# Performance work log

Measured on AMD Instinct MI355X. Metric: run time of the kernel, lower is better.

## Reference

```python
import math
import jax, jax.numpy as jnp
import numpy as np
from jax import lax

B, H, W, C1, D, NH = 32, 28, 28, 64, 256, 8
KS, RATIO = 9, 0.0005
NEG = -1.0e9


def setup_inputs() -> dict:
    key = jax.random.key(0)
    ks = jax.random.split(key, 6)
    x = jax.random.normal(ks[0], (B, 1, H, W), jnp.float32)
    conv_w = jax.random.normal(ks[1], (C1, 1, KS, KS), jnp.float32) * 0.05
    channel_embed = jax.random.normal(ks[2], (C1, D), jnp.float32)
    in_proj_w = jax.random.normal(ks[3], (3 * D, D), jnp.float32) * (1.0 / math.sqrt(D))
    in_proj_b = jnp.zeros((3 * D,), jnp.float32)
    out_proj_w = jax.random.normal(ks[4], (D, D), jnp.float32) * (1.0 / math.sqrt(D))
    out_proj_b = jnp.zeros((D,), jnp.float32)
    return {"x": x, "conv_w": conv_w, "channel_embed": channel_embed,
            "in_proj_w": in_proj_w, "in_proj_b": in_proj_b,
            "out_proj_w": out_proj_w, "out_proj_b": out_proj_b}


def _pos_encoding_2d(h, w, dim):
    # even dims: sin(y * div), odd dims: cos(x * div)  (matches torch broadcast)
    div = jnp.exp(jnp.arange(0, dim, 2, dtype=jnp.float32) * (-math.log(10000.0) / dim))
    pe_even = jnp.sin(jnp.arange(h, dtype=jnp.float32)[:, None] * div)  # (h, dim/2)
    pe_odd = jnp.cos(jnp.arange(w, dtype=jnp.float32)[:, None] * div)   # (w, dim/2)
    pe = jnp.zeros((h, w, dim), jnp.float32)
    pe = pe.at[..., 0::2].set(jnp.broadcast_to(pe_even[:, None, :], (h, w, dim // 2)))
    pe = pe.at[..., 1::2].set(jnp.broadcast_to(pe_odd[None, :, :], (h, w, dim // 2)))
    return pe


def reference(x, conv_w, channel_embed, in_proj_w, in_proj_b, out_proj_w, out_proj_b):
    pad = KS // 2
    A = jax.nn.relu(lax.conv_general_dilated(
        x, conv_w, (1, 1), [(pad, pad), (pad, pad)],
        dimension_numbers=("NCHW", "OIHW", "NCHW")))  # (B, C1, H, W)

    # global top-k threshold (kthvalue equivalent)
    total = A.size
    k = max(1, int(math.ceil(RATIO * total)))
    if k >= total:
        mask_global = jnp.ones_like(A, dtype=bool)
    else:
        vals, _ = lax.top_k(A.reshape(-1), k)
        mask_global = A >= vals[-1]
    A_g = A * mask_global.astype(A.dtype)

    v = jnp.transpose(A_g, (0, 2, 3, 1))  # (B, H, W, C1)
    nz = v > 0
    count = nz.sum(axis=-1)  # (B, H, W)

    top2_vals, top2_idx = lax.top_k(v, 2)  # (B,H,W,2)
    cidx = jnp.arange(C1)
    sel2 = (cidx == top2_idx[..., 0:1]) | (cidx == top2_idx[..., 1:2])
    idx_single = jnp.argmax(jnp.where(nz, v, -jnp.inf), axis=-1)
    sel1 = cidx == idx_single[..., None]

    logits = jnp.where((count >= 2)[..., None] & sel2, v, NEG)
    logits = jnp.where((count == 1)[..., None] & sel1, v, logits)
    sparse_weights = jax.nn.softmax(logits, axis=-1)
    sparse_weights = jnp.where((count == 0)[..., None], 0.0, sparse_weights)

    loc_emb = jnp.einsum("bhwc,cd->bhwd", sparse_weights, channel_embed)
    loc_emb = loc_emb + _pos_encoding_2d(H, W, D)[None]
    seq = loc_emb.reshape(B, H * W, D)

    # torch nn.MultiheadAttention (batch_first, self-attn)
    qkv = seq @ in_proj_w.T + in_proj_b  # (B, S, 3D)
    q, kk, vv = jnp.split(qkv, 3, axis=-1)
    hd = D // NH
    def heads(t):
        return t.reshape(B, H * W, NH, hd).transpose(0, 2, 1, 3)  # (B, NH, S, hd)
    q, kk, vv = heads(q), heads(kk), heads(vv)
    scores = jnp.einsum("bnqd,bnkd->bnqk", q, kk) / math.sqrt(hd)
    attn = jax.nn.softmax(scores, axis=-1)
    ctx = jnp.einsum("bnqk,bnkd->bnqd", attn, vv)
    ctx = ctx.transpose(0, 2, 1, 3).reshape(B, H * W, D)
    attn_out = ctx @ out_proj_w.T + out_proj_b
    pooled = attn_out.mean(axis=1)  # (B, D)
    return pooled, sparse_weights, top2_idx
```

## Files before the change

### kernel.cpp

```cpp
#include <hip/hip_runtime.h>
#include <cmath>

#define NB 32
#define C1N 64
#define DIM 256
#define NHEAD 8
#define SEQL 784
#define NA 1605632
#define SEQN 6422528
#define KSEL 803u
#define QK2S (0.17677669529663687f * 1.4426950408889634f)
#define THR2 11.541560f
#define PECOEF (-0.03597789207803197f)

#define AS1 __attribute__((address_space(1)))
#define AS3 __attribute__((address_space(3)))

typedef __attribute__((ext_vector_type(8))) short bf16x8;
typedef __attribute__((ext_vector_type(4))) float f32x4;

__device__ __forceinline__ unsigned short f2b(float f) {
  unsigned u = __float_as_uint(f);
  unsigned r = u + 0x7fffu + ((u >> 16) & 1u);
  return (unsigned short)(r >> 16);
}

__device__ __forceinline__ unsigned cvt_pk_bf16(float lo, float hi) {
  unsigned r;
  asm("v_cvt_pk_bf16_f32 %0, %1, %2" : "=v"(r) : "v"(lo), "v"(hi));
  return r;
}

__device__ __forceinline__ void scan256_suffix(unsigned* ss, int t) {
  #pragma unroll
  for (int off = 1; off < 256; off <<= 1) {
    unsigned v = (t + off < 256) ? ss[t + off] : 0u;
    __syncthreads();
    ss[t] += v;
    __syncthreads();
  }
}

__global__ __launch_bounds__(256) void k_init(const float* __restrict__ ipw,
                                              unsigned short* __restrict__ wbuf,
                                              unsigned* __restrict__ z) {
  int i = blockIdx.x * 256 + threadIdx.x;
  if (i < 66080) z[i] = 0u;
  wbuf[i] = f2b(ipw[i]);
}

__global__ __launch_bounds__(256) void k_conv(const float* __restrict__ x,
                                              const float* __restrict__ cw,
                                              float* __restrict__ vbuf,
                                              unsigned* __restrict__ hist8a) {
  __shared__ __align__(16) float ximg[1296];
  __shared__ float wlds[5184];
  __shared__ unsigned lh[256];
  int tid = threadIdx.x;
  int b = blockIdx.x / 7, sblk = blockIdx.x % 7;
  lh[tid] = 0u;
  for (int e = tid; e < 1296; e += 256) ximg[e] = 0.f;
  for (int e = tid; e < 5184; e += 256) {
    int c = e / 81, t = e - c * 81;
    wlds[t * 64 + c] = cw[e];
  }
  __syncthreads();
  const float* xb = x + b * 784;
  for (int e = tid; e < 784; e += 256) {
    int row = e / 28, col = e - row * 28;
    ximg[(row + 4) * 36 + col + 4] = xb[e];
  }
  __syncthreads();
  int wv = tid >> 6, lane = tid & 63;
  for (int it = 0; it < 7; ++it) {
    int grp = sblk * 28 + it * 4 + wv;
    int hr = grp / 7, wc0 = (grp % 7) * 4;
    float a0 = 0.f, a1 = 0.f, a2 = 0.f, a3 = 0.f;
    #pragma unroll
    for (int dy = 0; dy < 9; ++dy) {
      const float4* xr4 = (const float4*)&ximg[(hr + dy) * 36 + wc0];
      float4 xa = xr4[0], xbq = xr4[1], xc = xr4[2];
      float xr[12] = {xa.x, xa.y, xa.z, xa.w, xbq.x, xbq.y, xbq.z, xbq.w,
                      xc.x, xc.y, xc.z, xc.w};
      #pragma unroll
      for (int dx = 0; dx < 9; ++dx) {
        float w = wlds[(dy * 9 + dx) * 64 + lane];
        a0 = fmaf(xr[dx + 0], w, a0);
        a1 = fmaf(xr[dx + 1], w, a1);
        a2 = fmaf(xr[dx + 2], w, a2);
        a3 = fmaf(xr[dx + 3], w, a3);
      }
    }
    a0 = fmaxf(a0, 0.f); a1 = fmaxf(a1, 0.f);
    a2 = fmaxf(a2, 0.f); a3 = fmaxf(a3, 0.f);
    size_t base = ((size_t)(b * 784 + hr * 28 + wc0)) * 64 + lane;
    vbuf[base +   0] = a0;
    vbuf[base +  64] = a1;
    vbuf[base + 128] = a2;
    vbuf[base + 192] = a3;
    if (a0 > 0.f) atomicAdd(&lh[__float_as_uint(a0) >> 24], 1u);
    if (a1 > 0.f) atomicAdd(&lh[__float_as_uint(a1) >> 24], 1u);
    if (a2 > 0.f) atomicAdd(&lh[__float_as_uint(a2) >> 24], 1u);
    if (a3 > 0.f) atomicAdd(&lh[__float_as_uint(a3) >> 24], 1u);
  }
  __syncthreads();
  if (lh[tid] > 0u) atomicAdd(&hist8a[tid], lh[tid]);
}

__global__ __launch_bounds__(256) void k_h8b(const float* __restrict__ vbuf,
                                             const unsigned* __restrict__ hist8a,
                                             unsigned* __restrict__ hist8b) {
  __shared__ unsigned ss[256];
  __shared__ unsigned lh[256];
  __shared__ unsigned bkey;
  int t = threadIdx.x;
  ss[t] = hist8a[t];
  lh[t] = 0u;
  __syncthreads();
  scan256_suffix(ss, t);
  if (ss[0] < KSEL) return;
  unsigned S = ss[t], ab = (t < 255) ? ss[t + 1] : 0u;
  if (S >= KSEL && ab < KSEL) bkey = (unsigned)t;
  __syncthreads();
  unsigned key = bkey;
  const float4* v4 = (const float4*)vbuf;
  int n4 = NA / 4;
  for (int i = blockIdx.x * 256 + t; i < n4; i += gridDim.x * 256) {
    float4 v = v4[i];
    float vv[4] = {v.x, v.y, v.z, v.w};
    #pragma unroll
    for (int j = 0; j < 4; ++j) {
      if (vv[j] > 0.0f) {
        unsigned bits = __float_as_uint(vv[j]);
        if ((bits >> 24) == key) atomicAdd(&lh[(bits >> 16) & 0xFFu], 1u);
      }
    }
  }
  __syncthreads();
  if (lh[t] > 0u) atomicAdd(&hist8b[t], lh[t]);
}

__global__ __launch_bounds__(256) void k_h16(const float* __restrict__ vbuf,
                                             const unsigned* __restrict__ hist8a,
                                             const unsigned* __restrict__ hist8b,
                                             unsigned* __restrict__ hist16) {
  __shared__ unsigned ss[256];
  __shared__ unsigned bk0, bk1, brem;
  int t = threadIdx.x;
  ss[t] = hist8a[t];
  __syncthreads();
  scan256_suffix(ss, t);
  if (ss[0] < KSEL) return;
  unsigned S = ss[t], ab = (t < 255) ? ss[t + 1] : 0u;
  if (S >= KSEL && ab < KSEL) { bk0 = (unsigned)t; brem = KSEL - ab; }
  __syncthreads();
  unsigned key0 = bk0, rem1 = brem;
  __syncthreads();
  ss[t] = hist8b[t];
  __syncthreads();
  scan256_suffix(ss, t);
  S = ss[t]; ab = (t < 255) ? ss[t + 1] : 0u;
  if (S >= rem1 && ab < rem1) bk1 = (unsigned)t;
  __syncthreads();
  unsigned key16 = (key0 << 8) | bk1;
  const float4* v4 = (const float4*)vbuf;
  int n4 = NA / 4;
  for (int i = blockIdx.x * 256 + t; i < n4; i += gridDim.x * 256) {
    float4 v = v4[i];
    float vv[4] = {v.x, v.y, v.z, v.w};
    #pragma unroll
    for (int j = 0; j < 4; ++j) {
      if (vv[j] > 0.0f) {
        unsigned bits = __float_as_uint(vv[j]);
        if ((bits >> 16) == key16) atomicAdd(&hist16[bits & 0xFFFFu], 1u);
      }
    }
  }
}

__global__ __launch_bounds__(1024) void k_scan16(const unsigned* __restrict__ hist8a,
                                                 const unsigned* __restrict__ hist8b,
                                                 const unsigned* __restrict__ hist16,
                                                 unsigned* __restrict__ sel) {
  __shared__ unsigned ss[1024];
  __shared__ unsigned bk0, bk1, brem, brem2;
  int t = threadIdx.x;
  if (t < 256) ss[t] = hist8a[t];
  __syncthreads();
  for (int off = 1; off < 256; off <<= 1) {
    unsigned v = 0u;
    if (t < 256) v = (t + off < 256) ? ss[t + off] : 0u;
    __syncthreads();
    if (t < 256) ss[t] += v;
    __syncthreads();
  }
  if (ss[0] < KSEL) { if (t == 0) sel[3] = 0u; return; }
  if (t < 256) {
    unsigned S = ss[t], ab = (t < 255) ? ss[t + 1] : 0u;
    if (S >= KSEL && ab < KSEL) { bk0 = (unsigned)t; brem = KSEL - ab; }
  }
  __syncthreads();
  unsigned key0 = bk0, rem1 = brem;
  if (t < 256) ss[t] = hist8b[t];
  __syncthreads();
  for (int off = 1; off < 256; off <<= 1) {
    unsigned v = 0u;
    if (t < 256) v = (t + off < 256) ? ss[t + off] : 0u;
    __syncthreads();
    if (t < 256) ss[t] += v;
    __syncthreads();
  }
  if (t < 256) {
    unsigned S = ss[t], ab = (t < 255) ? ss[t + 1] : 0u;
    if (S >= rem1 && ab < rem1) { bk1 = (unsigned)t; brem2 = rem1 - ab; }
  }
  __syncthreads();
  unsigned key16 = (key0 << 8) | bk1;
  unsigned rem2 = brem2;
  unsigned sum = 0;
  for (int i = 0; i < 64; ++i) sum += hist16[t * 64 + i];
  ss[t] = sum;
  __syncthreads();
  for (int off = 1; off < 1024; off <<= 1) {
    unsigned v = (t + off < 1024) ? ss[t + off] : 0u;
    __syncthreads();
    ss[t] += v;
    __syncthreads();
  }
  unsigned S = ss[t];
  unsigned above = (t < 1023) ? ss[t + 1] : 0u;
  if (S >= rem2 && above < rem2) {
    unsigned cum = above;
    for (int bb = t * 64 + 63; bb >= t * 64; --bb) {
      unsigned hb = hist16[bb];
      cum += hb;
      if (cum >= rem2) {
        sel[3] = (key16 << 16) | (unsigned)bb;
        break;
      }
    }
  }
}

__global__ __launch_bounds__(256) void k_select(const float* __restrict__ vbuf,
                                                const unsigned* __restrict__ sel,
                                                const float* __restrict__ ce,
                                                unsigned short* __restrict__ seqb,
                                                float* __restrict__ out_sw,
                                                float* __restrict__ out_idx) {
  int wid = threadIdx.x >> 6;
  int lane = threadIdx.x & 63;
  int pos = blockIdx.x * 4 + wid;
  int hw = pos % 784;
  int hr = hw / 28;
  int wc = hw % 28;
  float thr = __uint_as_float(sel[3]);
  float a = vbuf[(size_t)pos * 64 + lane];
  float val = (a >= thr) ? a : 0.0f;
  unsigned long long nzm = __ballot(val > 0.0f);
  int count = __popcll(nzm);
  float v1 = val; int i1 = lane;
  #pragma unroll
  for (int off = 32; off > 0; off >>= 1) {
    float ov = __shfl_xor(v1, off);
    int oi = __shfl_xor(i1, off);
    if (ov > v1 || (ov == v1 && oi < i1)) { v1 = ov; i1 = oi; }
  }
  float vx = (lane == i1) ? -INFINITY : val;
  float v2 = vx; int i2 = lane;
  #pragma unroll
  for (int off = 32; off > 0; off >>= 1) {
    float ov = __shfl_xor(v2, off);
    int oi = __shfl_xor(i2, off);
    if (ov > v2 || (ov == v2 && oi < i2)) { v2 = ov; i2 = oi; }
  }
  float w1 = 0.0f, w2 = 0.0f;
  if (count >= 2) {
    float e = __expf(v2 - v1);
    float invd = 1.0f / (1.0f + e);
    w1 = invd; w2 = e * invd;
  } else if (count == 1) {
    w1 = 1.0f;
  }
  float wt = (lane == i1) ? w1 : ((lane == i2) ? w2 : 0.0f);
  out_sw[(size_t)pos * 64 + lane] = wt;
  if (lane < 2) out_idx[pos * 2 + lane] = (float)(lane == 0 ? i1 : i2);
  int d0 = lane * 4;
  float4 c1v = *(const float4*)(ce + (size_t)i1 * 256 + d0);
  float4 c2v = *(const float4*)(ce + (size_t)i2 * 256 + d0);
  float dv0 = __expf((float)d0 * PECOEF);
  float dv2 = __expf((float)(d0 + 2) * PECOEF);
  float ox = w1 * c1v.x + w2 * c2v.x + __sinf((float)hr * dv0);
  float oy = w1 * c1v.y + w2 * c2v.y + __cosf((float)wc * dv0);
  float oz = w1 * c1v.z + w2 * c2v.z + __sinf((float)hr * dv2);
  float ow = w1 * c1v.w + w2 * c2v.w + __cosf((float)wc * dv2);
  ushort4 ob = make_ushort4(f2b(ox), f2b(oy), f2b(oz), f2b(ow));
  *(ushort4*)(seqb + (size_t)pos * 256 + d0) = ob;
}

__global__ __launch_bounds__(256) void k_gemm_lds(const unsigned short* __restrict__ A,
                                                  const unsigned short* __restrict__ W,
                                                  const float* __restrict__ bias,
                                                  unsigned short* __restrict__ C,
                                                  unsigned short* __restrict__ Vt,
                                                  int M, int N, int K) {
  __shared__ __align__(16) unsigned short As[8192];
  __shared__ __align__(16) unsigned short Bs[8192];
  int tid = threadIdx.x;
  int lane = tid & 63, wid = tid >> 6;
  int q = lane & 15, g = lane >> 4;
  int m0 = blockIdx.y * 128, n0 = blockIdx.x * 128;
  int lrow = lane >> 3, s = lane & 7;
  const unsigned short* aSrc = A + (size_t)(m0 + wid * 8 + lrow) * K + (s ^ lrow) * 8;
  const unsigned short* bSrc = W + (size_t)(n0 + wid * 8 + lrow) * K + (s ^ lrow) * 8;
  int dstW = wid * 512;
  int mloc = (wid >> 1) * 64, nloc = (wid & 1) * 64;
  int q7 = q & 7;
  f32x4 acc[4][4];
  #pragma unroll
  for (int i = 0; i < 4; ++i)
    #pragma unroll
    for (int j = 0; j < 4; ++j) acc[i][j] = (f32x4){0.f, 0.f, 0.f, 0.f};
  for (int k0 = 0; k0 < K; k0 += 64) {
    #pragma unroll
    for (int i = 0; i < 4; ++i) {
      __builtin_amdgcn_global_load_lds((const AS1 void*)(aSrc + (size_t)i * 32 * K + k0),
                                       (AS3 void*)(&As[i * 2048 + dstW]), 16, 0, 0);
      __builtin_amdgcn_global_load_lds((const AS1 void*)(bSrc + (size_t)i * 32 * K + k0),
                                       (AS3 void*)(&Bs[i * 2048 + dstW]), 16, 0, 0);
    }
    __syncthreads();
    #pragma unroll
    for (int kk = 0; kk < 2; ++kk) {
      bf16x8 af[4], bf[4];
      #pragma unroll
      for (int i = 0; i < 4; ++i)
        af[i] = *(const bf16x8*)&As[(mloc + i * 16 + q) * 64 + (((kk * 4 + g) ^ q7) * 8)];
      #pragma unroll
      for (int j = 0; j < 4; ++j)
        bf[j] = *(const bf16x8*)&Bs[(nloc + j * 16 + q) * 64 + (((kk * 4 + g) ^ q7) * 8)];
      __builtin_amdgcn_s_setprio(1);
      #pragma unroll
      for (int i = 0; i < 4; ++i)
        #pragma unroll
        for (int j = 0; j < 4; ++j)
          acc[i][j] = __builtin_amdgcn_mfma_f32_16x16x32_bf16(af[i], bf[j], acc[i][j], 0, 0, 0);
      __builtin_amdgcn_s_setprio(0);
    }
    __syncthreads();
  }
  if (n0 < 512) {
    #pragma unroll
    for (int j = 0; j < 4; ++j) {
      int col = n0 + nloc + j * 16 + q;
      float bj = bias[col];
      float qs = (col < 256) ? QK2S : 1.0f;
      #pragma unroll
      for (int i = 0; i < 4; ++i) {
        #pragma unroll
        for (int r = 0; r < 4; ++r) {
          int row = m0 + mloc + i * 16 + g * 4 + r;
          C[(size_t)row * N + col] = f2b((acc[i][j][r] + bj) * qs);
        }
      }
    }
  } else {
    #pragma unroll
    for (int j = 0; j < 4; ++j) {
      int colV = n0 + nloc + j * 16 + q;
      float bj = bias[colV];
      int dtot = colV - 512;
      size_t vrow = ((size_t)(dtot >> 5) * 32 + (dtot & 31)) * 800;
      #pragma unroll
      for (int i = 0; i < 4; ++i) {
        int rowbase = m0 + mloc + i * 16;
        int b = rowbase / 784;
        int t16 = rowbase - b * 784;
        int pos = ((t16 >> 5) << 5) + ((t16 >> 4) & 1) * 4 + g * 8;
        uint2 o;
        o.x = cvt_pk_bf16(acc[i][j][0] + bj, acc[i][j][1] + bj);
        o.y = cvt_pk_bf16(acc[i][j][2] + bj, acc[i][j][3] + bj);
        *(uint2*)(Vt + (size_t)b * 8 * 32 * 800 + vrow + pos) = o;
      }
    }
  }
}

__global__ __launch_bounds__(256) void k_attn(const unsigned short* __restrict__ qkv,
                                              const unsigned short* __restrict__ Vt,
                                              unsigned short* __restrict__ ctx) {
  __shared__ __align__(16) unsigned short Kt[3][1024];
  __shared__ __align__(16) unsigned short Vti[3][1024];
  int wid = threadIdx.x >> 6;
  int lane = threadIdx.x & 63;
  int blk = blockIdx.x;
  int wrk = (blk & 7) * 416 + (blk >> 3);
  int bh = wrk / 13;
  int qb = (wrk - bh * 13) * 4 + wid;
  int b = bh >> 3, nh = bh & 7;
  int q = lane & 15, g = lane >> 4;
  bool active = (qb < 49);
  const f32x4 zero4 = {0.f, 0.f, 0.f, 0.f};

  int qrow = b * 784 + (active ? qb * 16 + q : q);
  bf16x8 qf = *(const bf16x8*)(qkv + (size_t)qrow * 768 + nh * 32 + g * 8);
  asm volatile("s_waitcnt vmcnt(0)" ::: "memory");

  const unsigned short* kbase = qkv + (size_t)b * 784 * 768 + 256 + nh * 32;
  const unsigned short* vbase = Vt + (size_t)bh * 32 * 800;

  int rit = ((wid & 1) << 4) + (lane >> 2);
  int sG = (lane & 3) ^ ((rit + (rit >> 2)) & 3);
  bool isK = (wid < 2);
  int ldsoff = ((wid & 1) << 4) * 32;
  const unsigned short* sp = isK ? (kbase + (size_t)rit * 768 + sG * 8)
                                 : (vbase + (size_t)rit * 800 + sG * 8);
  const int sstride = isK ? (32 * 768) : 32;
  unsigned short* ldsb = (isK ? &Kt[0][0] : &Vti[0][0]) + ldsoff;

  int slotr = ((g ^ ((q + (q >> 2)) & 3)) << 3);
  int rowA = q * 32 + slotr;
  int rowB = (16 + q) * 32 + slotr;

  f32x4 acc0 = zero4, acc1 = zero4;
  float m = -INFINITY, lp = 0.f;

#define STAGE(BUFO) {                                                          \
    __builtin_amdgcn_global_load_lds((const AS1 void*)sp,                      \
                                     (AS3 void*)(ldsb + (BUFO)), 16, 0, 0);    \
    sp += sstride; }

#define STEP(CUR, NXT) {                                                       \
    asm volatile("s_waitcnt vmcnt(1)" ::: "memory");                           \
    __builtin_amdgcn_s_barrier();                                              \
    asm volatile("" ::: "memory");                                             \
    STAGE(NXT);                                                                \
    bf16x8 kA = *(const bf16x8*)&Kt[0][(CUR) + rowA];                          \
    bf16x8 kB = *(const bf16x8*)&Kt[0][(CUR) + rowB];                          \
    bf16x8 va = *(const bf16x8*)&Vti[0][(CUR) + rowA];                         \
    bf16x8 vb = *(const bf16x8*)&Vti[0][(CUR) + rowB];                         \
    __builtin_amdgcn_s_setprio(1);                                             \
    f32x4 s0 = __builtin_amdgcn_mfma_f32_16x16x32_bf16(kA, qf, zero4, 0, 0, 0);\
    f32x4 s1 = __builtin_amdgcn_mfma_f32_16x16x32_bf16(kB, qf, zero4, 0, 0, 0);\
    __builtin_amdgcn_s_setprio(0);                                             \
    float pl = fmaxf(fmaxf(fmaxf(s0[0], s0[1]), fmaxf(s0[2], s0[3])),          \
                     fmaxf(fmaxf(s1[0], s1[1]), fmaxf(s1[2], s1[3])));         \
    if (!__all(pl <= m + THR2)) {                                              \
      float pm = fmaxf(pl, __shfl_xor(pl, 16));                                \
      pm = fmaxf(pm, __shfl_xor(pm, 32));                                      \
      float mnew = fmaxf(m, pm);                                               \
      float sc = __builtin_amdgcn_exp2f(m - mnew);                             \
      lp *= sc; acc0 *= sc; acc1 *= sc;                                        \
      m = mnew;                                                                \
    }                                                                          \
    float p0[4], p1[4];                                                        \
    _Pragma("unroll")                                                          \
    for (int r = 0; r < 4; ++r) {                                              \
      p0[r] = __builtin_amdgcn_exp2f(s0[r] - m);                               \
      p1[r] = __builtin_amdgcn_exp2f(s1[r] - m);                               \
    }                                                                          \
    lp += ((p0[0] + p0[1]) + (p0[2] + p0[3]))                                  \
        + ((p1[0] + p1[1]) + (p1[2] + p1[3]));                                 \
    union { unsigned u[4]; bf16x8 v; } pu;                                     \
    pu.u[0] = cvt_pk_bf16(p0[0], p0[1]);                                       \
    pu.u[1] = cvt_pk_bf16(p0[2], p0[3]);                                       \
    pu.u[2] = cvt_pk_bf16(p1[0], p1[1]);                                       \
    pu.u[3] = cvt_pk_bf16(p1[2], p1[3]);                                       \
    __builtin_amdgcn_s_setprio(1);                                             \
    acc0 = __builtin_amdgcn_mfma_f32_16x16x32_bf16(va, pu.v, acc0, 0, 0, 0);   \
    acc1 = __builtin_amdgcn_mfma_f32_16x16x32_bf16(vb, pu.v, acc1, 0, 0, 0);   \
    __builtin_amdgcn_s_setprio(0);                                             \
  }

  STAGE(0);
  STAGE(1024);

  for (int t = 0; t < 8; ++t) {
    STEP(0, 2048);
    STEP(1024, 0);
    STEP(2048, 1024);
  }
  {
    asm volatile("s_waitcnt vmcnt(1)" ::: "memory");
    __builtin_amdgcn_s_barrier();
    asm volatile("" ::: "memory");
    bf16x8 kA = *(const bf16x8*)&Kt[0][rowA];
    bf16x8 va = *(const bf16x8*)&Vti[0][rowA];
    bf16x8 vb = *(const bf16x8*)&Vti[0][rowB];
    f32x4 s0 = __builtin_amdgcn_mfma_f32_16x16x32_bf16(kA, qf, zero4, 0, 0, 0);
    float pl = fmaxf(fmaxf(s0[0], s0[1]), fmaxf(s0[2], s0[3]));
    if (!__all(pl <= m + THR2)) {
      float pm = fmaxf(pl, __shfl_xor(pl, 16));
      pm = fmaxf(pm, __shfl_xor(pm, 32));
      float mnew = fmaxf(m, pm);
      float sc = __builtin_amdgcn_exp2f(m - mnew);
      lp *= sc; acc0 *= sc; acc1 *= sc;
      m = mnew;
    }
    float p0[4];
    #pragma unroll
    for (int r = 0; r < 4; ++r) p0[r] = __builtin_amdgcn_exp2f(s0[r] - m);
    lp += (p0[0] + p0[1]) + (p0[2] + p0[3]);
    union { unsigned u[4]; bf16x8 v; } pu;
    pu.u[0] = cvt_pk_bf16(p0[0], p0[1]);
    pu.u[1] = cvt_pk_bf16(p0[2], p0[3]);
    pu.u[2] = 0u;
    pu.u[3] = 0u;
    acc0 = __builtin_amdgcn_mfma_f32_16x16x32_bf16(va, pu.v, acc0, 0, 0, 0);
    acc1 = __builtin_amdgcn_mfma_f32_16x16x32_bf16(vb, pu.v, acc1, 0, 0, 0);
  }
#undef STEP
#undef STAGE
  float l = lp + __shfl_xor(lp, 16);
  l += __shfl_xor(l, 32);
  float linv = 1.f / l;
  if (active) {
    unsigned short* cp = ctx + (size_t)(b * 784 + qb * 16 + q) * 256 + nh * 32;
    ushort4 oA = make_ushort4(f2b(acc0[0] * linv), f2b(acc0[1] * linv),
                              f2b(acc0[2] * linv), f2b(acc0[3] * linv));
    ushort4 oB = make_ushort4(f2b(acc1[0] * linv), f2b(acc1[1] * linv),
                              f2b(acc1[2] * linv), f2b(acc1[3] * linv));
    *(ushort4*)(cp + g * 4) = oA;
    *(ushort4*)(cp + 16 + g * 4) = oB;
  }
}

__global__ __launch_bounds__(256) void k_poolctx(const unsigned short* __restrict__ ctx,
                                                 float* __restrict__ part) {
  int b = blockIdx.x >> 3, sseg = blockIdx.x & 7;
  int d = threadIdx.x;
  const unsigned short* base = ctx + ((size_t)b * 784 + sseg * 98) * 256 + d;
  float acc = 0.f;
  for (int t = 0; t < 98; ++t)
    acc += __uint_as_float((unsigned)base[(size_t)t * 256] << 16);
  part[(size_t)blockIdx.x * 256 + d] = acc;
}

__global__ __launch_bounds__(256) void k_pgemv(const float* __restrict__ part,
                                               const float* __restrict__ opw,
                                               const float* __restrict__ opb,
                                               float* __restrict__ out) {
  __shared__ float mc[256];
  int b = blockIdx.x, d = threadIdx.x;
  float s = 0.f;
  #pragma unroll
  for (int i = 0; i < 8; ++i) s += part[(size_t)(b * 8 + i) * 256 + d];
  mc[d] = s * (1.0f / 784.0f);
  __syncthreads();
  float acc = opb[d];
  const float4* wr = (const float4*)(opw + (size_t)d * 256);
  #pragma unroll 8
  for (int j = 0; j < 64; ++j) {
    float4 w = wr[j];
    float4 m4 = *(const float4*)&mc[j * 4];
    acc += m4.x * w.x + m4.y * w.y + m4.z * w.z + m4.w * w.w;
  }
  out[b * 256 + d] = acc;
}

extern "C" void kernel_launch(void* const* d_in, const int* in_sizes, int n_in,
                              void* d_out, int out_size, void* d_ws, size_t ws_size,
                              hipStream_t stream) {
  (void)in_sizes; (void)n_in; (void)out_size; (void)ws_size;
  const float* x   = (const float*)d_in[0];
  const float* cw  = (const float*)d_in[1];
  const float* ce  = (const float*)d_in[2];
  const float* ipw = (const float*)d_in[3];
  const float* ipb = (const float*)d_in[4];
  const float* opw = (const float*)d_in[5];
  const float* opb = (const float*)d_in[6];

  float* out = (float*)d_out;
  float* pooled  = out;
  float* out_sw  = out + 8192;
  float* out_idx = out + 8192 + NA;

  float* ws = (float*)d_ws;
  float* vbuf = ws;
  unsigned* hist16 = (unsigned*)(ws + NA);
  unsigned* hist8a = hist16 + 65536;
  unsigned* hist8b = hist8a + 256;
  unsigned* sel    = hist8b + 256;
  unsigned short* seqb = (unsigned short*)(ws + NA + 66080);
  unsigned short* qkvb = seqb + SEQN;
  unsigned short* Vt   = qkvb + 3 * (size_t)SEQN;
  unsigned short* wbuf = Vt + 256 * 32 * 800;
  float* part = (float*)(wbuf + 262144);

  k_init<<<768, 256, 0, stream>>>(ipw, wbuf, hist16);
  k_conv<<<224, 256, 0, stream>>>(x, cw, vbuf, hist8a);
  k_h8b<<<1024, 256, 0, stream>>>(vbuf, hist8a, hist8b);
  k_h16<<<1024, 256, 0, stream>>>(vbuf, hist8a, hist8b, hist16);
  k_scan16<<<1, 1024, 0, stream>>>(hist8a, hist8b, hist16, sel);
  k_select<<<25088 / 4, 256, 0, stream>>>(vbuf, sel, ce, seqb, out_sw, out_idx);
  {
    dim3 gq(768 / 128, 25088 / 128);
    k_gemm_lds<<<gq, 256, 0, stream>>>(seqb, wbuf, ipb, qkvb, Vt, 25088, 768, 256);
  }
  k_attn<<<3328, 256, 0, stream>>>(qkvb, Vt, seqb );
  k_poolctx<<<256, 256, 0, stream>>>(seqb, part);
  k_pgemv<<<NB, 256, 0, stream>>>(part, opw, opb, pooled);
}
```

Before: 164.8 us.

## Compute softmax row sums via MFMA with ones and fuse pooling with output GEMV

In the attention kernel the per-lane scalar sum of probabilities and its final cross-lane shuffles are replaced by an extra MFMA against an all-ones bf16 vector, so the denominator comes out of the matrix unit already reduced. The max computation is also reordered into a shallower three-way form. The separate pooling and output-GEMV kernels are merged into one 1024-thread-per-batch kernel that reduces across segments through shared memory, saving a launch and a workspace round trip. The row sum is now taken from bf16-rounded probabilities, which slightly changes numerics. The fused kernel also runs only 32 blocks, which lowers parallelism in the pooling read.

```diff
diff --git a/kernel.cpp b/kernel.cpp
--- a/kernel.cpp
+++ b/kernel.cpp
@@ -401,6 +401,9 @@
   int q = lane & 15, g = lane >> 4;
   bool active = (qb < 49);
   const f32x4 zero4 = {0.f, 0.f, 0.f, 0.f};
+  const short one_bf = (short)0x3F80;
+  const bf16x8 ones8 = {one_bf, one_bf, one_bf, one_bf,
+                        one_bf, one_bf, one_bf, one_bf};
 
   int qrow = b * 784 + (active ? qb * 16 + q : q);
   bf16x8 qf = *(const bf16x8*)(qkv + (size_t)qrow * 768 + nh * 32 + g * 8);
@@ -422,8 +425,8 @@
   int rowA = q * 32 + slotr;
   int rowB = (16 + q) * 32 + slotr;
 
-  f32x4 acc0 = zero4, acc1 = zero4;
-  float m = -INFINITY, lp = 0.f;
+  f32x4 acc0 = zero4, acc1 = zero4, accS = zero4;
+  float m = -INFINITY;
 
 #define STAGE(BUFO) {                                                          \
     __builtin_amdgcn_global_load_lds((const AS1 void*)sp,                      \
@@ -443,14 +446,16 @@
     f32x4 s0 = __builtin_amdgcn_mfma_f32_16x16x32_bf16(kA, qf, zero4, 0, 0, 0);\
     f32x4 s1 = __builtin_amdgcn_mfma_f32_16x16x32_bf16(kB, qf, zero4, 0, 0, 0);\
     __builtin_amdgcn_s_setprio(0);                                             \
-    float pl = fmaxf(fmaxf(fmaxf(s0[0], s0[1]), fmaxf(s0[2], s0[3])),          \
-                     fmaxf(fmaxf(s1[0], s1[1]), fmaxf(s1[2], s1[3])));         \
+    float t1 = fmaxf(fmaxf(s0[0], s0[1]), s0[2]);                              \
+    float t2 = fmaxf(fmaxf(s0[3], s1[0]), s1[1]);                              \
+    float t3 = fmaxf(fmaxf(s1[2], s1[3]), t1);                                 \
+    float pl = fmaxf(t2, t3);                                                  \
     if (!__all(pl <= m + THR2)) {                                              \
       float pm = fmaxf(pl, __shfl_xor(pl, 16));                                \
       pm = fmaxf(pm, __shfl_xor(pm, 32));                                      \
       float mnew = fmaxf(m, pm);                                               \
       float sc = __builtin_amdgcn_exp2f(m - mnew);                             \
-      lp *= sc; acc0 *= sc; acc1 *= sc;                                        \
+      acc0 *= sc; acc1 *= sc; accS *= sc;                                      \
       m = mnew;                                                                \
     }                                                                          \
     float p0[4], p1[4];                                                        \
@@ -459,8 +464,6 @@
       p0[r] = __builtin_amdgcn_exp2f(s0[r] - m);                               \
       p1[r] = __builtin_amdgcn_exp2f(s1[r] - m);                               \
     }                                                                          \
-    lp += ((p0[0] + p0[1]) + (p0[2] + p0[3]))                                  \
-        + ((p1[0] + p1[1]) + (p1[2] + p1[3]));                                 \
     union { unsigned u[4]; bf16x8 v; } pu;                                     \
     pu.u[0] = cvt_pk_bf16(p0[0], p0[1]);                                       \
     pu.u[1] = cvt_pk_bf16(p0[2], p0[3]);                                       \
@@ -469,6 +472,7 @@
     __builtin_amdgcn_s_setprio(1);                                             \
     acc0 = __builtin_amdgcn_mfma_f32_16x16x32_bf16(va, pu.v, acc0, 0, 0, 0);   \
     acc1 = __builtin_amdgcn_mfma_f32_16x16x32_bf16(vb, pu.v, acc1, 0, 0, 0);   \
+    accS = __builtin_amdgcn_mfma_f32_16x16x32_bf16(ones8, pu.v, accS, 0, 0, 0);\
     __builtin_amdgcn_s_setprio(0);                                             \
   }
 
@@ -488,19 +492,18 @@
     bf16x8 va = *(const bf16x8*)&Vti[0][rowA];
     bf16x8 vb = *(const bf16x8*)&Vti[0][rowB];
     f32x4 s0 = __builtin_amdgcn_mfma_f32_16x16x32_bf16(kA, qf, zero4, 0, 0, 0);
-    float pl = fmaxf(fmaxf(s0[0], s0[1]), fmaxf(s0[2], s0[3]));
+    float pl = fmaxf(fmaxf(fmaxf(s0[0], s0[1]), s0[2]), s0[3]);
     if (!__all(pl <= m + THR2)) {
       float pm = fmaxf(pl, __shfl_xor(pl, 16));
       pm = fmaxf(pm, __shfl_xor(pm, 32));
       float mnew = fmaxf(m, pm);
       float sc = __builtin_amdgcn_exp2f(m - mnew);
-      lp *= sc; acc0 *= sc; acc1 *= sc;
+      acc0 *= sc; acc1 *= sc; accS *= sc;
       m = mnew;
     }
     float p0[4];
     #pragma unroll
     for (int r = 0; r < 4; ++r) p0[r] = __builtin_amdgcn_exp2f(s0[r] - m);
-    lp += (p0[0] + p0[1]) + (p0[2] + p0[3]);
     union { unsigned u[4]; bf16x8 v; } pu;
     pu.u[0] = cvt_pk_bf16(p0[0], p0[1]);
     pu.u[1] = cvt_pk_bf16(p0[2], p0[3]);
@@ -508,12 +511,11 @@
     pu.u[3] = 0u;
     acc0 = __builtin_amdgcn_mfma_f32_16x16x32_bf16(va, pu.v, acc0, 0, 0, 0);
     acc1 = __builtin_amdgcn_mfma_f32_16x16x32_bf16(vb, pu.v, acc1, 0, 0, 0);
+    accS = __builtin_amdgcn_mfma_f32_16x16x32_bf16(ones8, pu.v, accS, 0, 0, 0);
   }
 #undef STEP
 #undef STAGE
-  float l = lp + __shfl_xor(lp, 16);
-  l += __shfl_xor(l, 32);
-  float linv = 1.f / l;
+  float linv = 1.f / accS[0];
   if (active) {
     unsigned short* cp = ctx + (size_t)(b * 784 + qb * 16 + q) * 256 + nh * 32;
     ushort4 oA = make_ushort4(f2b(acc0[0] * linv), f2b(acc0[1] * linv),
@@ -525,37 +527,36 @@
   }
 }
 
-__global__ __launch_bounds__(256) void k_poolctx(const unsigned short* __restrict__ ctx,
-                                                 float* __restrict__ part) {
-  int b = blockIdx.x >> 3, sseg = blockIdx.x & 7;
-  int d = threadIdx.x;
-  const unsigned short* base = ctx + ((size_t)b * 784 + sseg * 98) * 256 + d;
+__global__ __launch_bounds__(1024) void k_poolgemv(const unsigned short* __restrict__ ctx,
+                                                   const float* __restrict__ opw,
+                                                   const float* __restrict__ opb,
+                                                   float* __restrict__ out) {
+  __shared__ float red[4][256];
+  __shared__ float mc[256];
+  int b = blockIdx.x;
+  int d = threadIdx.x & 255;
+  int seg = threadIdx.x >> 8;
+  const unsigned short* base = ctx + ((size_t)b * 784 + seg * 196) * 256 + d;
   float acc = 0.f;
-  for (int t = 0; t < 98; ++t)
+  for (int t = 0; t < 196; ++t)
     acc += __uint_as_float((unsigned)base[(size_t)t * 256] << 16);
-  part[(size_t)blockIdx.x * 256 + d] = acc;
-}
-
-__global__ __launch_bounds__(256) void k_pgemv(const float* __restrict__ part,
-                                               const float* __restrict__ opw,
-                                               const float* __restrict__ opb,
-                                               float* __restrict__ out) {
-  __shared__ float mc[256];
-  int b = blockIdx.x, d = threadIdx.x;
-  float s = 0.f;
-  #pragma unroll
-  for (int i = 0; i < 8; ++i) s += part[(size_t)(b * 8 + i) * 256 + d];
-  mc[d] = s * (1.0f / 784.0f);
-  __syncthreads();
-  float acc = opb[d];
-  const float4* wr = (const float4*)(opw + (size_t)d * 256);
-  #pragma unroll 8
-  for (int j = 0; j < 64; ++j) {
+  red[seg][d] = acc;
+  __syncthreads();
+  if (seg == 0)
+    mc[d] = (red[0][d] + red[1][d] + red[2][d] + red[3][d]) * (1.0f / 784.0f);
+  __syncthreads();
+  float ap = 0.f;
+  const float4* wr = (const float4*)(opw + (size_t)d * 256 + seg * 64);
+  #pragma unroll 4
+  for (int j = 0; j < 16; ++j) {
     float4 w = wr[j];
-    float4 m4 = *(const float4*)&mc[j * 4];
-    acc += m4.x * w.x + m4.y * w.y + m4.z * w.z + m4.w * w.w;
-  }
-  out[b * 256 + d] = acc;
+    float4 m4 = *(const float4*)&mc[seg * 64 + j * 4];
+    ap += m4.x * w.x + m4.y * w.y + m4.z * w.z + m4.w * w.w;
+  }
+  red[seg][d] = ap;
+  __syncthreads();
+  if (seg == 0)
+    out[b * 256 + d] = red[0][d] + red[1][d] + red[2][d] + red[3][d] + opb[d];
 }
 
 extern "C" void kernel_launch(void* const* d_in, const int* in_sizes, int n_in,
@@ -585,7 +586,6 @@
   unsigned short* qkvb = seqb + SEQN;
   unsigned short* Vt   = qkvb + 3 * (size_t)SEQN;
   unsigned short* wbuf = Vt + 256 * 32 * 800;
-  float* part = (float*)(wbuf + 262144);
 
   k_init<<<768, 256, 0, stream>>>(ipw, wbuf, hist16);
   k_conv<<<224, 256, 0, stream>>>(x, cw, vbuf, hist8a);
@@ -598,6 +598,5 @@
     k_gemm_lds<<<gq, 256, 0, stream>>>(seqb, wbuf, ipb, qkvb, Vt, 25088, 768, 256);
   }
   k_attn<<<3328, 256, 0, stream>>>(qkvb, Vt, seqb );
-  k_poolctx<<<256, 256, 0, stream>>>(seqb, part);
-  k_pgemv<<<NB, 256, 0, stream>>>(part, opw, opb, pooled);
-}
+  k_poolgemv<<<NB, 1024, 0, stream>>>(seqb, opw, opb, pooled);
+}
```

New measurement: 164.7 us. Within noise of the previous version (-0.0%).
